# Performance work log

Hardware: AMD Instinct MI355X
Metric: run time of the kernel (lower is better)

## Reference

```python
import jax, jax.numpy as jnp
import numpy as np

DIM = 2048
N_HEADS = 16
HEAD_DIM = DIM // N_HEADS
ROPE_BASE = 10000


def l2norm(x, axis=-1, eps=1e-12):
    n = jnp.sqrt(jnp.sum(x * x, axis=axis, keepdims=True))
    return x / jnp.maximum(n, eps)


def rope_tables(T, dim, base, dtype):
    theta = 1.0 / (base ** (jnp.arange(0, dim, 2, dtype=dtype) / dim))  # [dim/2]
    ang = jnp.arange(T, dtype=dtype)[:, None] * theta[None, :]          # [T, dim/2]
    return jnp.sin(ang), jnp.cos(ang)


def apply_rope(x, sin, cos):
    # x: [B, H, T, D]; sin/cos: [T, D/2] (half-split convention, not interleaved)
    half = x.shape[-1] // 2
    xr, xi = x[..., :half], x[..., half:]
    yr = xr * cos - xi * sin
    yi = xr * sin + xi * cos
    return jnp.concatenate([yr, yi], axis=-1)


def setup_inputs() -> dict:
    key = jax.random.key(0)
    ks = jax.random.split(key, 5)
    B, T = 1, 2048
    x = jax.random.normal(ks[0], (B, T, DIM), dtype=jnp.float32)
    wq = jax.random.normal(ks[1], (DIM, DIM), dtype=jnp.float32) * 0.02
    wk = jax.random.normal(ks[2], (DIM, DIM), dtype=jnp.float32) * 0.02
    wv = jax.random.normal(ks[3], (DIM, DIM), dtype=jnp.float32) * 0.02
    wo = jax.random.normal(ks[4], (DIM, DIM), dtype=jnp.float32) * 0.02
    sqk = jnp.ones((N_HEADS, 1, HEAD_DIM), dtype=jnp.float32) * (1.0 / DIM ** 0.5)
    return {"x": x, "wq": wq, "wk": wk, "wv": wv, "wo": wo, "sqk": sqk}


def reference(x, wq, wk, wv, wo, sqk):
    B, T, C = x.shape
    H, D = N_HEADS, HEAD_DIM
    restore = C ** 0.5  # restore_scale_sqk = sqkinit / sqkscale
    actual_sqk = sqk * restore  # [H, 1, D]

    def proj(w):
        return jnp.einsum('btc,oc->bto', x, w).reshape(B, T, H, D).transpose(0, 2, 1, 3)

    q = proj(wq)  # [B, H, T, D]
    new_k = proj(wk)
    new_v = proj(wv)

    sin, cos = rope_tables(T, D, ROPE_BASE, x.dtype)
    q = apply_rope(q, sin, cos) * actual_sqk
    k = apply_rope(new_k, sin, cos) * actual_sqk

    # NOTE: original uses scale=head_dim**0.5 (multiplies by sqrt(D))
    scores = jnp.einsum('bhqd,bhkd->bhqk', q, k) * (D ** 0.5)
    mask = jnp.tril(jnp.ones((T, T), dtype=bool))
    scores = jnp.where(mask, scores, jnp.finfo(scores.dtype).min)
    attn = jax.nn.softmax(scores, axis=-1)
    out = jnp.einsum('bhqk,bhkd->bhqd', attn, new_v)  # [B, H, T, D]
    out = out.transpose(0, 2, 1, 3).reshape(B, T, C)
    out = jnp.einsum('btc,oc->bto', out, wo)
    return (l2norm(out), (new_k, new_v))
```

## Files before the change

### kernel.cpp

```cpp
#include <hip/hip_runtime.h>

typedef __bf16 bf16x8 __attribute__((ext_vector_type(8)));
typedef float f32x4 __attribute__((ext_vector_type(4)));
typedef unsigned short us4 __attribute__((ext_vector_type(4)));

constexpr int TT = 2048;
constexpr int CC = 2048;
constexpr int HH = 16;
constexpr int DD = 128;

__device__ __forceinline__ unsigned short f2bf(float f) {
  unsigned u = __builtin_bit_cast(unsigned, f);
  u += 0x7FFFu + ((u >> 16) & 1u);
  return (unsigned short)(u >> 16);
}
__device__ __forceinline__ float bf2f(unsigned short b) {
  unsigned u = ((unsigned)b) << 16;
  return __builtin_bit_cast(float, u);
}

__device__ __forceinline__ void gld_lds16(const unsigned short* g, unsigned short* l) {
  __builtin_amdgcn_global_load_lds(
      (const __attribute__((address_space(1))) unsigned int*)g,
      (__attribute__((address_space(3))) unsigned int*)l,
      16, 0, 0);
}

__global__ __launch_bounds__(256) void k_cvt5(
    const float* __restrict__ s0, const float* __restrict__ s1,
    const float* __restrict__ s2, const float* __restrict__ s3,
    const float* __restrict__ s4,
    unsigned short* __restrict__ d0, unsigned short* __restrict__ d1,
    unsigned short* __restrict__ d2, unsigned short* __restrict__ d3,
    unsigned short* __restrict__ d4) {
  const int m = blockIdx.y;
  const float* src = (m == 0) ? s0 : (m == 1) ? s1 : (m == 2) ? s2 : (m == 3) ? s3 : s4;
  unsigned short* dst = (m == 0) ? d0 : (m == 1) ? d1 : (m == 2) ? d2 : (m == 3) ? d3 : d4;
  int i = blockIdx.x * 256 + threadIdx.x;
  const float4* s = (const float4*)src;
  float4 a = s[2 * i], b = s[2 * i + 1];
  us4 lo = { f2bf(a.x), f2bf(a.y), f2bf(a.z), f2bf(a.w) };
  us4 hi = { f2bf(b.x), f2bf(b.y), f2bf(b.z), f2bf(b.w) };
  us4* d = (us4*)dst;
  d[2 * i] = lo;
  d[2 * i + 1] = hi;
}

#define WAIT_LGKM0                                      \
  asm volatile("s_waitcnt lgkmcnt(0)" ::: "memory");    \
  __builtin_amdgcn_sched_barrier(0);
#define BAR __builtin_amdgcn_s_barrier();

__global__ __launch_bounds__(512, 2) void k_gemm192(
    const unsigned short* __restrict__ A, const unsigned short* __restrict__ B,
    unsigned short* __restrict__ qraw,
    float* __restrict__ outk, float* __restrict__ outv) {
  __shared__ alignas(16) unsigned short As[2][256 * 64];
  __shared__ alignas(16) unsigned short Bs[2][192 * 64];
  const int K = CC, NT = K >> 6, NT2 = NT >> 1;
  const int tid = threadIdx.x;
  const int m0 = blockIdx.y * 256, n0 = blockIdx.x * 192;
  const int wid = tid >> 6, lane = tid & 63;
  const int wr = wid >> 2, wc = wid & 3;
  const int lr = lane & 15, lg = lane >> 4;

  auto stA = [&](int buf, int jb, int tile) {
#pragma unroll
    for (int j = jb; j < jb + 2; ++j) {
      const int ch = tid + j * 512;
      const int r = ch >> 3, c8 = ch & 7;
      gld_lds16(A + (size_t)(m0 + r) * K + tile * 64 + ((c8 ^ (r & 7)) * 8),
                &As[buf][ch * 8]);
    }
  };
  auto stB2 = [&](int buf, int tile) {
#pragma unroll
    for (int j = 0; j < 2; ++j) {
      const int ch = tid + j * 512;
      const int r = ch >> 3, c8 = ch & 7;
      gld_lds16(B + (size_t)(n0 + r) * K + tile * 64 + ((c8 ^ (r & 7)) * 8),
                &Bs[buf][ch * 8]);
    }
  };
  auto stB1 = [&](int buf, int tile) {
    const int ch = tid + 1024;
    const int r = ch >> 3, c8 = ch & 7;
    gld_lds16(B + (size_t)(n0 + r) * K + tile * 64 + ((c8 ^ (r & 7)) * 8),
              &Bs[buf][ch * 8]);
  };

  f32x4 acc[8][3] = {};
  bf16x8 alo[4][2], ahi[4][2], b01[2][2], b2v[2];

  auto rdAlo = [&](int d) {
#pragma unroll
    for (int im = 0; im < 4; ++im)
#pragma unroll
      for (int kk = 0; kk < 2; ++kk) {
        const int row = wr * 128 + im * 16 + lr;
        alo[im][kk] = *(const bf16x8*)(&As[d][row * 64 + (((kk * 4 + lg) ^ (row & 7)) * 8)]);
      }
  };
  auto rdAhi = [&](int d) {
#pragma unroll
    for (int im = 0; im < 4; ++im)
#pragma unroll
      for (int kk = 0; kk < 2; ++kk) {
        const int row = wr * 128 + (4 + im) * 16 + lr;
        ahi[im][kk] = *(const bf16x8*)(&As[d][row * 64 + (((kk * 4 + lg) ^ (row & 7)) * 8)]);
      }
  };
  auto rdB01 = [&](int d) {
#pragma unroll
    for (int in = 0; in < 2; ++in)
#pragma unroll
      for (int kk = 0; kk < 2; ++kk) {
        const int row = wc * 48 + in * 16 + lr;
        b01[in][kk] = *(const bf16x8*)(&Bs[d][row * 64 + (((kk * 4 + lg) ^ (row & 7)) * 8)]);
      }
  };
  auto rdB2 = [&](int d) {
#pragma unroll
    for (int kk = 0; kk < 2; ++kk) {
      const int row = wc * 48 + 32 + lr;
      b2v[kk] = *(const bf16x8*)(&Bs[d][row * 64 + (((kk * 4 + lg) ^ (row & 7)) * 8)]);
    }
  };

  auto q_lo01 = [&]() {
    __builtin_amdgcn_s_setprio(1);
#pragma unroll
    for (int im = 0; im < 4; ++im)
#pragma unroll
      for (int in = 0; in < 2; ++in)
#pragma unroll
        for (int kk = 0; kk < 2; ++kk)
          acc[im][in] = __builtin_amdgcn_mfma_f32_16x16x32_bf16(alo[im][kk], b01[in][kk], acc[im][in], 0, 0, 0);
    __builtin_amdgcn_s_setprio(0);
  };
  auto q_lo2 = [&]() {
    __builtin_amdgcn_s_setprio(1);
#pragma unroll
    for (int im = 0; im < 4; ++im)
#pragma unroll
      for (int kk = 0; kk < 2; ++kk)
        acc[im][2] = __builtin_amdgcn_mfma_f32_16x16x32_bf16(alo[im][kk], b2v[kk], acc[im][2], 0, 0, 0);
    __builtin_amdgcn_s_setprio(0);
  };
  auto q_hi2 = [&]() {
    __builtin_amdgcn_s_setprio(1);
#pragma unroll
    for (int im = 0; im < 4; ++im)
#pragma unroll
      for (int kk = 0; kk < 2; ++kk)
        acc[4 + im][2] = __builtin_amdgcn_mfma_f32_16x16x32_bf16(ahi[im][kk], b2v[kk], acc[4 + im][2], 0, 0, 0);
    __builtin_amdgcn_s_setprio(0);
  };
  auto q_hi01 = [&]() {
    __builtin_amdgcn_s_setprio(1);
#pragma unroll
    for (int im = 0; im < 4; ++im)
#pragma unroll
      for (int in = 0; in < 2; ++in)
#pragma unroll
        for (int kk = 0; kk < 2; ++kk)
          acc[4 + im][in] = __builtin_amdgcn_mfma_f32_16x16x32_bf16(ahi[im][kk], b01[in][kk], acc[4 + im][in], 0, 0, 0);
    __builtin_amdgcn_s_setprio(0);
  };

  stB2(0, 0); stB1(0, 0); stA(0, 0, 0); stA(0, 2, 0);
  stB2(1, 1); stB1(1, 1);
  asm volatile("s_waitcnt vmcnt(3)" ::: "memory");
  __builtin_amdgcn_sched_barrier(0);
  BAR

  for (int t = 0; t < NT2; ++t) {
    const int t1 = 2 * t + 1, t2 = 2 * t + 2, t3 = 2 * t + 3;
    const bool s2 = t2 < NT;

    rdAlo(0); rdB01(0);
    stA(1, 0, t1);
    BAR WAIT_LGKM0
    q_lo01();
    BAR
    rdB2(0);
    stA(1, 2, t1);
    BAR WAIT_LGKM0
    q_lo2();
    BAR
    rdAhi(0);
    if (s2) stB2(0, t2);
    BAR WAIT_LGKM0
    q_hi2();
    BAR
    if (s2) stB1(0, t2);
    q_hi01();
    if (s2) { asm volatile("s_waitcnt vmcnt(3)" ::: "memory"); }
    else    { asm volatile("s_waitcnt vmcnt(0)" ::: "memory"); }
    __builtin_amdgcn_sched_barrier(0);
    BAR

    rdAlo(1); rdB01(1);
    if (s2) stA(0, 0, t2);
    BAR WAIT_LGKM0
    q_lo01();
    BAR
    rdB2(1);
    if (s2) stA(0, 2, t2);
    BAR WAIT_LGKM0
    q_lo2();
    BAR
    rdAhi(1);
    if (s2) stB2(1, t3);
    BAR WAIT_LGKM0
    q_hi2();
    BAR
    if (s2) stB1(1, t3);
    q_hi01();
    if (s2) { asm volatile("s_waitcnt vmcnt(3)" ::: "memory"); }
    else    { asm volatile("s_waitcnt vmcnt(0)" ::: "memory"); }
    __builtin_amdgcn_sched_barrier(0);
    BAR
  }

#pragma unroll
  for (int mf = 0; mf < 8; ++mf) {
    const int row = m0 + wr * 128 + mf * 16 + lg * 4;
#pragma unroll
    for (int nf = 0; nf < 3; ++nf) {
      const int col = n0 + wc * 48 + nf * 16 + lr;
#pragma unroll
      for (int r = 0; r < 4; ++r) {
        float v = acc[mf][nf][r];
        int rr = row + r;
        if (col < 2048) {
          qraw[(size_t)rr * 2048 + col] = f2bf(v);
        } else if (col < 4096) {
          int c = col - 2048;
          outk[(size_t)(c >> 7) * (TT * DD) + (size_t)rr * DD + (c & 127)] = v;
        } else {
          int c = col - 4096;
          outv[(size_t)(c >> 7) * (TT * DD) + (size_t)rr * DD + (c & 127)] = v;
        }
      }
    }
  }
}

__global__ __launch_bounds__(512, 2) void k_gemm8p(
    const unsigned short* __restrict__ A, const unsigned short* __restrict__ B,
    int N, int K, int kspan,
    float* __restrict__ out0, float* __restrict__ out1,
    float* __restrict__ out2, float* __restrict__ out3) {
  __shared__ alignas(16) unsigned short As[2][2][128 * 64];
  __shared__ alignas(16) unsigned short Bs[2][2][128 * 64];
  const int tid = threadIdx.x;
  const int m0 = blockIdx.y * 256, n0 = blockIdx.x * 256;
  const int kbeg = blockIdx.z * kspan;
  const int NT = kspan >> 6, NT2 = NT >> 1;
  const int wid = tid >> 6, lane = tid & 63;
  const int wr = wid >> 2, wc = wid & 3;
  const int lr = lane & 15, lg = lane >> 4;
  const int bh = wc >> 1, brow0 = (wc & 1) * 64;

  const int sr0 = tid >> 3, sc0 = tid & 7;
  const unsigned short* Ab = A + kbeg;
  const unsigned short* Bb = B + kbeg;

  auto stageA = [&](int buf, int half, int tile) {
    const int koff = tile * 64;
#pragma unroll
    for (int j = 0; j < 2; ++j) {
      const int r = sr0 + j * 64;
      gld_lds16(Ab + (size_t)(m0 + half * 128 + r) * K + koff + ((sc0 ^ (r & 7)) * 8),
                &As[buf][half][(tid + j * 512) * 8]);
    }
  };
  auto stageB = [&](int buf, int half, int tile) {
    const int koff = tile * 64;
#pragma unroll
    for (int j = 0; j < 2; ++j) {
      const int r = sr0 + j * 64;
      gld_lds16(Bb + (size_t)(n0 + half * 128 + r) * K + koff + ((sc0 ^ (r & 7)) * 8),
                &Bs[buf][half][(tid + j * 512) * 8]);
    }
  };

  f32x4 acc[8][4] = {};
  bf16x8 alo[4][2], ahi[4][2], ba[2][2], bb[2][2];

  auto rdAlo = [&](int d) {
#pragma unroll
    for (int im = 0; im < 4; ++im)
#pragma unroll
      for (int kk = 0; kk < 2; ++kk) {
        const int row = im * 16 + lr;
        alo[im][kk] = *(const bf16x8*)(&As[d][wr][row * 64 + (((kk * 4 + lg) ^ (row & 7)) * 8)]);
      }
  };
  auto rdAhi = [&](int d) {
#pragma unroll
    for (int im = 0; im < 4; ++im)
#pragma unroll
      for (int kk = 0; kk < 2; ++kk) {
        const int row = (4 + im) * 16 + lr;
        ahi[im][kk] = *(const bf16x8*)(&As[d][wr][row * 64 + (((kk * 4 + lg) ^ (row & 7)) * 8)]);
      }
  };
  auto rdBa = [&](int d) {
#pragma unroll
    for (int in = 0; in < 2; ++in)
#pragma unroll
      for (int kk = 0; kk < 2; ++kk) {
        const int row = brow0 + in * 16 + lr;
        ba[in][kk] = *(const bf16x8*)(&Bs[d][bh][row * 64 + (((kk * 4 + lg) ^ (row & 7)) * 8)]);
      }
  };
  auto rdBb = [&](int d) {
#pragma unroll
    for (int in = 0; in < 2; ++in)
#pragma unroll
      for (int kk = 0; kk < 2; ++kk) {
        const int row = brow0 + (2 + in) * 16 + lr;
        bb[in][kk] = *(const bf16x8*)(&Bs[d][bh][row * 64 + (((kk * 4 + lg) ^ (row & 7)) * 8)]);
      }
  };

#define MFMA_Q(MB, NB, AF, BF)                                                     \
  __builtin_amdgcn_s_setprio(1);                                                   \
  _Pragma("unroll") for (int im = 0; im < 4; ++im)                                 \
      _Pragma("unroll") for (int in = 0; in < 2; ++in)                             \
          _Pragma("unroll") for (int kk = 0; kk < 2; ++kk)                         \
              acc[MB + im][NB + in] = __builtin_amdgcn_mfma_f32_16x16x32_bf16(     \
                  AF[im][kk], BF[in][kk], acc[MB + im][NB + in], 0, 0, 0);         \
  __builtin_amdgcn_s_setprio(0);

  stageB(0, 0, 0); stageB(0, 1, 0); stageA(0, 0, 0); stageA(0, 1, 0);
  if (NT > 1) { stageB(1, 0, 1); stageB(1, 1, 1); }
  asm volatile("s_waitcnt vmcnt(4)" ::: "memory");
  __builtin_amdgcn_sched_barrier(0);
  BAR

  for (int t = 0; t < NT2; ++t) {
    const int t1 = 2 * t + 1, t2 = 2 * t + 2, t3 = 2 * t + 3;
    const bool s2 = t2 < NT, s3 = t3 < NT;

    rdAlo(0); rdBa(0);
    stageA(1, 0, t1);
    BAR WAIT_LGKM0
    MFMA_Q(0, 0, alo, ba)
    BAR
    rdBb(0);
    stageA(1, 1, t1);
    BAR WAIT_LGKM0
    MFMA_Q(0, 2, alo, bb)
    BAR
    rdAhi(0);
    if (s2) stageB(0, 0, t2);
    BAR WAIT_LGKM0
    MFMA_Q(4, 2, ahi, bb)
    BAR
    if (s2) stageB(0, 1, t2);
    MFMA_Q(4, 0, ahi, ba)
    if (s2) { asm volatile("s_waitcnt vmcnt(4)" ::: "memory"); }
    else    { asm volatile("s_waitcnt vmcnt(0)" ::: "memory"); }
    __builtin_amdgcn_sched_barrier(0);
    BAR

    rdAlo(1); rdBa(1);
    if (s2) stageA(0, 0, t2);
    BAR WAIT_LGKM0
    MFMA_Q(0, 0, alo, ba)
    BAR
    rdBb(1);
    if (s2) stageA(0, 1, t2);
    BAR WAIT_LGKM0
    MFMA_Q(0, 2, alo, bb)
    BAR
    rdAhi(1);
    if (s3) stageB(1, 0, t3);
    BAR WAIT_LGKM0
    MFMA_Q(4, 2, ahi, bb)
    BAR
    if (s3) stageB(1, 1, t3);
    MFMA_Q(4, 0, ahi, ba)
    if (s3) { asm volatile("s_waitcnt vmcnt(4)" ::: "memory"); }
    else    { asm volatile("s_waitcnt vmcnt(0)" ::: "memory"); }
    __builtin_amdgcn_sched_barrier(0);
    BAR
  }
#undef MFMA_Q

  int z = blockIdx.z;
  float* dst = (z == 0) ? out0 : (z == 1) ? out1 : (z == 2) ? out2 : out3;
#pragma unroll
  for (int mf = 0; mf < 8; ++mf) {
    const int row = m0 + wr * 128 + mf * 16 + lg * 4;
#pragma unroll
    for (int nf = 0; nf < 4; ++nf) {
      const int col = n0 + wc * 64 + nf * 16 + lr;
#pragma unroll
      for (int r = 0; r < 4; ++r) {
        dst[(size_t)(row + r) * N + col] = acc[mf][nf][r];
      }
    }
  }
}
#undef WAIT_LGKM0
#undef BAR

__global__ __launch_bounds__(256) void k_rope(
    const unsigned short* __restrict__ qraw, const float* __restrict__ Kraw,
    const float* __restrict__ sqk,
    unsigned short* __restrict__ qb, unsigned short* __restrict__ kb) {
  const int t = blockIdx.x;
  for (int i = threadIdx.x; i < HH * 64; i += 256) {
    int h = i >> 6, dp = i & 63;
    float theta = expf(-(float)dp * 0.14391156831212787f);
    float ang = (float)t * theta;
    float sn, cs;
    sincosf(ang, &sn, &cs);
    float qr = bf2f(qraw[(size_t)t * CC + h * DD + dp]);
    float qi = bf2f(qraw[(size_t)t * CC + h * DD + dp + 64]);
    const float* kp = Kraw + (size_t)h * TT * DD + (size_t)t * DD;
    float kr = kp[dp], ki = kp[dp + 64];
    float sr = sqk[h * DD + dp];
    float si = sqk[h * DD + dp + 64];
    float qsr = sr * 512.0f, qsi = si * 512.0f;
    float ksr = sr * 45.25483399593904f, ksi = si * 45.25483399593904f;
    unsigned short* qo = qb + ((size_t)h * TT + t) * DD;
    unsigned short* ko = kb + ((size_t)h * TT + t) * DD;
    qo[dp]      = f2bf((qr * cs - qi * sn) * qsr);
    qo[dp + 64] = f2bf((qr * sn + qi * cs) * qsi);
    ko[dp]      = f2bf((kr * cs - ki * sn) * ksr);
    ko[dp + 64] = f2bf((kr * sn + ki * cs) * ksi);
  }
}

__global__ __launch_bounds__(256) void k_vt(
    const float* __restrict__ Vraw, unsigned short* __restrict__ vt) {
  const int h = blockIdx.z;
  const int t0 = blockIdx.x * 64, d0 = blockIdx.y * 64;
  __shared__ unsigned short tile[64][65];
  const float* vp = Vraw + (size_t)h * TT * DD;
  for (int i = threadIdx.x; i < 4096; i += 256) {
    int r = i >> 6, c = i & 63;
    tile[r][c] = f2bf(vp[(size_t)(t0 + r) * DD + d0 + c]);
  }
  __syncthreads();
  unsigned short* op = vt + (size_t)h * DD * TT;
  for (int i = threadIdx.x; i < 4096; i += 256) {
    int dr = i >> 6, tc = i & 63;
    op[(size_t)(d0 + dr) * TT + t0 + tc] = tile[tc][dr];
  }
}

__global__ __launch_bounds__(512) void k_attn_pair(
    const unsigned short* __restrict__ qb, const unsigned short* __restrict__ kb,
    const unsigned short* __restrict__ vt, unsigned short* __restrict__ ob) {
  const int gA = blockIdx.x, h = blockIdx.y;
  const int gB = 31 - gA;
  const int ntiles = gB + 1;
  const int tid = threadIdx.x;
  const int wid = tid >> 6, lane = tid & 63;
  const int lr = lane & 15, lg = lane >> 4;
  const int gq = (wid >> 2) ? gB : gA;
  const int q0 = gq * 64 + (wid & 3) * 16;

  __shared__ alignas(16) unsigned short Ks[2][64 * 128];
  __shared__ alignas(16) unsigned short Vs[2][128 * 64];
  __shared__ alignas(16) unsigned short P[8][16][72];

  const unsigned short* qh = qb + (size_t)h * TT * DD;
  const unsigned short* kh = kb + (size_t)h * TT * DD;
  const unsigned short* vh = vt + (size_t)h * DD * TT;

  auto stageKV = [&](int buf, int kt) {
    const int k0 = kt * 64;
#pragma unroll
    for (int half = 0; half < 2; ++half) {
      int ch = tid + half * 512;
      int r = ch >> 4, c4 = ch & 15;
      gld_lds16(kh + (size_t)(k0 + r) * DD + ((c4 ^ (r & 7)) * 8), Ks[buf] + ch * 8);
    }
#pragma unroll
    for (int half = 0; half < 2; ++half) {
      int ch = tid + half * 512;
      int d = ch >> 3, c8 = ch & 7;
      gld_lds16(vh + (size_t)d * TT + k0 + ((c8 ^ (d & 7)) * 8), Vs[buf] + ch * 8);
    }
  };

  bf16x8 qf[4];
#pragma unroll
  for (int c = 0; c < 4; ++c)
    qf[c] = *(const bf16x8*)(qh + (size_t)(q0 + lr) * DD + c * 32 + lg * 8);

  f32x4 acc[8] = {};
  float mrow[4] = {-3e38f, -3e38f, -3e38f, -3e38f};
  float lsum[4] = {0.f, 0.f, 0.f, 0.f};

  stageKV(0, 0);
  asm volatile("s_waitcnt vmcnt(0)" ::: "memory");
  __builtin_amdgcn_sched_barrier(0);
  __builtin_amdgcn_s_barrier();

  for (int kt = 0; kt < ntiles; ++kt) {
    const int cur = kt & 1;
    const int k0 = kt * 64;
    if (kt + 1 < ntiles) stageKV(cur ^ 1, kt + 1);

    if (k0 <= q0 + 15) {
      f32x4 sv[4] = {};
#pragma unroll
      for (int ktile = 0; ktile < 4; ++ktile) {
        const int row = ktile * 16 + lr;
#pragma unroll
        for (int c = 0; c < 4; ++c) {
          int chn = (c * 4 + lg) ^ (lr & 7);
          bf16x8 kf = *(const bf16x8*)(Ks[cur] + row * 128 + chn * 8);
          sv[ktile] = __builtin_amdgcn_mfma_f32_16x16x32_bf16(qf[c], kf, sv[ktile], 0, 0, 0);
        }
      }
      if (k0 + 63 > q0) {
#pragma unroll
        for (int ktile = 0; ktile < 4; ++ktile)
#pragma unroll
          for (int r = 0; r < 4; ++r) {
            int key = k0 + ktile * 16 + lr;
            int qrow = q0 + lg * 4 + r;
            if (key > qrow) sv[ktile][r] = -1e30f;
          }
      }
      float pmax[4];
#pragma unroll
      for (int r = 0; r < 4; ++r)
        pmax[r] = fmaxf(fmaxf(sv[0][r], sv[1][r]), fmaxf(sv[2][r], sv[3][r]));
#pragma unroll
      for (int msk = 1; msk <= 8; msk <<= 1)
#pragma unroll
        for (int r = 0; r < 4; ++r) pmax[r] = fmaxf(pmax[r], __shfl_xor(pmax[r], msk));
      float p[4][4], ps[4], scl[4];
#pragma unroll
      for (int r = 0; r < 4; ++r) {
        float mn = fmaxf(mrow[r], pmax[r]);
        scl[r] = __expf(mrow[r] - mn);
        mrow[r] = mn;
        ps[r] = 0.f;
#pragma unroll
        for (int ktile = 0; ktile < 4; ++ktile) {
          p[ktile][r] = __expf(sv[ktile][r] - mn);
          ps[r] += p[ktile][r];
        }
      }
#pragma unroll
      for (int msk = 1; msk <= 8; msk <<= 1)
#pragma unroll
        for (int r = 0; r < 4; ++r) ps[r] += __shfl_xor(ps[r], msk);
#pragma unroll
      for (int r = 0; r < 4; ++r) lsum[r] = lsum[r] * scl[r] + ps[r];
#pragma unroll
      for (int n = 0; n < 8; ++n)
#pragma unroll
        for (int r = 0; r < 4; ++r) acc[n][r] *= scl[r];
#pragma unroll
      for (int ktile = 0; ktile < 4; ++ktile)
#pragma unroll
        for (int r = 0; r < 4; ++r)
          P[wid][lg * 4 + r][ktile * 16 + lr] = f2bf(p[ktile][r]);
      asm volatile("s_waitcnt lgkmcnt(0)" ::: "memory");
      __builtin_amdgcn_sched_barrier(0);
      bf16x8 pf[2];
#pragma unroll
      for (int ks = 0; ks < 2; ++ks)
        pf[ks] = *(const bf16x8*)(&P[wid][lr][ks * 32 + lg * 8]);
#pragma unroll
      for (int n = 0; n < 8; ++n) {
        const int row = n * 16 + lr;
#pragma unroll
        for (int ks = 0; ks < 2; ++ks) {
          int chn = (ks * 4 + lg) ^ (lr & 7);
          bf16x8 vf = *(const bf16x8*)(Vs[cur] + row * 64 + chn * 8);
          acc[n] = __builtin_amdgcn_mfma_f32_16x16x32_bf16(pf[ks], vf, acc[n], 0, 0, 0);
        }
      }
    }
    asm volatile("s_waitcnt vmcnt(0)" ::: "memory");
    __builtin_amdgcn_sched_barrier(0);
    __builtin_amdgcn_s_barrier();
  }

  float inv[4];
#pragma unroll
  for (int r = 0; r < 4; ++r) inv[r] = 1.0f / lsum[r];
#pragma unroll
  for (int n = 0; n < 8; ++n)
#pragma unroll
    for (int r = 0; r < 4; ++r) {
      int t = q0 + lg * 4 + r;
      ob[(size_t)t * CC + h * DD + n * 16 + lr] = f2bf(acc[n][r] * inv[r]);
    }
}

__global__ __launch_bounds__(256) void k_l2norm(
    const float* __restrict__ Of0, const float* __restrict__ Of1,
    const float* __restrict__ Of2, const float* __restrict__ Of3,
    float* __restrict__ out) {
  const int t = blockIdx.x;
  const int tid = threadIdx.x;
  const float4* p0 = (const float4*)(Of0 + (size_t)t * CC);
  const float4* p1 = (const float4*)(Of1 + (size_t)t * CC);
  const float4* p2 = (const float4*)(Of2 + (size_t)t * CC);
  const float4* p3 = (const float4*)(Of3 + (size_t)t * CC);
  float4 a = p0[2 * tid], b = p0[2 * tid + 1];
  float4 a1 = p1[2 * tid], b1 = p1[2 * tid + 1];
  float4 a2 = p2[2 * tid], b2 = p2[2 * tid + 1];
  float4 a3 = p3[2 * tid], b3 = p3[2 * tid + 1];
  a.x += a1.x + a2.x + a3.x; a.y += a1.y + a2.y + a3.y;
  a.z += a1.z + a2.z + a3.z; a.w += a1.w + a2.w + a3.w;
  b.x += b1.x + b2.x + b3.x; b.y += b1.y + b2.y + b3.y;
  b.z += b1.z + b2.z + b3.z; b.w += b1.w + b2.w + b3.w;
  float ss = a.x * a.x + a.y * a.y + a.z * a.z + a.w * a.w +
             b.x * b.x + b.y * b.y + b.z * b.z + b.w * b.w;
#pragma unroll
  for (int msk = 1; msk < 64; msk <<= 1) ss += __shfl_xor(ss, msk);
  __shared__ float red[4];
  if ((tid & 63) == 0) red[tid >> 6] = ss;
  __syncthreads();
  ss = red[0] + red[1] + red[2] + red[3];
  float sc = 1.0f / fmaxf(sqrtf(ss), 1e-12f);
  float4 oa = { a.x * sc, a.y * sc, a.z * sc, a.w * sc };
  float4 obv = { b.x * sc, b.y * sc, b.z * sc, b.w * sc };
  float4* o = (float4*)(out + (size_t)t * CC);
  o[2 * tid] = oa;
  o[2 * tid + 1] = obv;
}

extern "C" void kernel_launch(void* const* d_in, const int* in_sizes, int n_in,
                              void* d_out, int out_size, void* d_ws, size_t ws_size,
                              hipStream_t stream) {
  const float* x   = (const float*)d_in[0];
  const float* wq  = (const float*)d_in[1];
  const float* wk  = (const float*)d_in[2];
  const float* wv  = (const float*)d_in[3];
  const float* wo  = (const float*)d_in[4];
  const float* sqk = (const float*)d_in[5];

  float* out_norm = (float*)d_out;
  float* out_k = out_norm + (size_t)4 * 1024 * 1024;
  float* out_v = out_norm + (size_t)8 * 1024 * 1024;

  char* ws = (char*)d_ws;
  unsigned short* xb  = (unsigned short*)(ws);
  unsigned short* w1b = (unsigned short*)(ws + (8u << 20));
  unsigned short* wob = (unsigned short*)(ws + (32u << 20));
  unsigned short* qb  = (unsigned short*)(ws + (40u << 20));
  unsigned short* kb  = (unsigned short*)(ws + (48u << 20));
  unsigned short* vtb = (unsigned short*)(ws + (56u << 20));
  unsigned short* obb = (unsigned short*)(ws + (64u << 20));
  unsigned short* qraw = (unsigned short*)(ws + (72u << 20));

  float* Of0 = (float*)(ws + (72u << 20));
  float* Of1 = (float*)(ws);
  float* Of2 = (float*)(ws + (16u << 20));
  float* Of3 = (float*)(ws + (40u << 20));

  k_cvt5<<<dim3(2048, 5), 256, 0, stream>>>(
      x, wq, wk, wv, wo,
      xb, w1b, w1b + (size_t)4 * 1024 * 1024, w1b + (size_t)8 * 1024 * 1024, wob);

  k_gemm192<<<dim3(32, 8), 512, 0, stream>>>(xb, w1b, qraw, out_k, out_v);

  k_rope<<<TT, 256, 0, stream>>>(qraw, out_k, sqk, qb, kb);
  k_vt<<<dim3(32, 2, 16), 256, 0, stream>>>(out_v, vtb);

  k_attn_pair<<<dim3(16, 16), 512, 0, stream>>>(qb, kb, vtb, obb);

  k_gemm8p<<<dim3(8, 8, 4), 512, 0, stream>>>(obb, wob, CC, CC, CC / 4,
                                              Of0, Of1, Of2, Of3);

  k_l2norm<<<TT, 256, 0, stream>>>(Of0, Of1, Of2, Of3, out_norm);
}
```

Baseline: 201.8 us.

## Fuse V transpose into QKV GEMM epilogue and store split-K partials in bf16

```diff
diff --git a/kernel.cpp b/kernel.cpp
--- a/kernel.cpp
+++ b/kernel.cpp
@@ -54,7 +54,8 @@
 __global__ __launch_bounds__(512, 2) void k_gemm192(
     const unsigned short* __restrict__ A, const unsigned short* __restrict__ B,
     unsigned short* __restrict__ qraw,
-    float* __restrict__ outk, float* __restrict__ outv) {
+    float* __restrict__ outk, float* __restrict__ outv,
+    unsigned short* __restrict__ vtb) {
   __shared__ alignas(16) unsigned short As[2][256 * 64];
   __shared__ alignas(16) unsigned short Bs[2][192 * 64];
   const int K = CC, NT = K >> 6, NT2 = NT >> 1;
@@ -229,19 +230,26 @@
 #pragma unroll
     for (int nf = 0; nf < 3; ++nf) {
       const int col = n0 + wc * 48 + nf * 16 + lr;
-#pragma unroll
-      for (int r = 0; r < 4; ++r) {
-        float v = acc[mf][nf][r];
-        int rr = row + r;
-        if (col < 2048) {
-          qraw[(size_t)rr * 2048 + col] = f2bf(v);
-        } else if (col < 4096) {
-          int c = col - 2048;
-          outk[(size_t)(c >> 7) * (TT * DD) + (size_t)rr * DD + (c & 127)] = v;
-        } else {
-          int c = col - 4096;
-          outv[(size_t)(c >> 7) * (TT * DD) + (size_t)rr * DD + (c & 127)] = v;
+      if (col < 2048) {
+#pragma unroll
+        for (int r = 0; r < 4; ++r)
+          qraw[(size_t)(row + r) * 2048 + col] = f2bf(acc[mf][nf][r]);
+      } else if (col < 4096) {
+        const int c = col - 2048;
+#pragma unroll
+        for (int r = 0; r < 4; ++r)
+          outk[(size_t)(c >> 7) * (TT * DD) + (size_t)(row + r) * DD + (c & 127)] = acc[mf][nf][r];
+      } else {
+        const int c = col - 4096;
+        const int hh = c >> 7, d2 = c & 127;
+        us4 tv;
+#pragma unroll
+        for (int r = 0; r < 4; ++r) {
+          float v = acc[mf][nf][r];
+          outv[(size_t)hh * (TT * DD) + (size_t)(row + r) * DD + d2] = v;
+          tv[r] = f2bf(v);
         }
+        *(us4*)(vtb + (size_t)hh * (size_t)(DD * TT) + (size_t)d2 * TT + row) = tv;
       }
     }
   }
@@ -250,8 +258,8 @@
 __global__ __launch_bounds__(512, 2) void k_gemm8p(
     const unsigned short* __restrict__ A, const unsigned short* __restrict__ B,
     int N, int K, int kspan,
-    float* __restrict__ out0, float* __restrict__ out1,
-    float* __restrict__ out2, float* __restrict__ out3) {
+    unsigned short* __restrict__ out0, unsigned short* __restrict__ out1,
+    unsigned short* __restrict__ out2, unsigned short* __restrict__ out3) {
   __shared__ alignas(16) unsigned short As[2][2][128 * 64];
   __shared__ alignas(16) unsigned short Bs[2][2][128 * 64];
   const int tid = threadIdx.x;
@@ -392,7 +400,7 @@
 #undef MFMA_Q
 
   int z = blockIdx.z;
-  float* dst = (z == 0) ? out0 : (z == 1) ? out1 : (z == 2) ? out2 : out3;
+  unsigned short* dst = (z == 0) ? out0 : (z == 1) ? out1 : (z == 2) ? out2 : out3;
 #pragma unroll
   for (int mf = 0; mf < 8; ++mf) {
     const int row = m0 + wr * 128 + mf * 16 + lg * 4;
@@ -401,7 +409,7 @@
       const int col = n0 + wc * 64 + nf * 16 + lr;
 #pragma unroll
       for (int r = 0; r < 4; ++r) {
-        dst[(size_t)(row + r) * N + col] = acc[mf][nf][r];
+        dst[(size_t)(row + r) * N + col] = f2bf(acc[mf][nf][r]);
       }
     }
   }
@@ -437,24 +445,6 @@
   }
 }
 
-__global__ __launch_bounds__(256) void k_vt(
-    const float* __restrict__ Vraw, unsigned short* __restrict__ vt) {
-  const int h = blockIdx.z;
-  const int t0 = blockIdx.x * 64, d0 = blockIdx.y * 64;
-  __shared__ unsigned short tile[64][65];
-  const float* vp = Vraw + (size_t)h * TT * DD;
-  for (int i = threadIdx.x; i < 4096; i += 256) {
-    int r = i >> 6, c = i & 63;
-    tile[r][c] = f2bf(vp[(size_t)(t0 + r) * DD + d0 + c]);
-  }
-  __syncthreads();
-  unsigned short* op = vt + (size_t)h * DD * TT;
-  for (int i = threadIdx.x; i < 4096; i += 256) {
-    int dr = i >> 6, tc = i & 63;
-    op[(size_t)(d0 + dr) * TT + t0 + tc] = tile[tc][dr];
-  }
-}
-
 __global__ __launch_bounds__(512) void k_attn_pair(
     const unsigned short* __restrict__ qb, const unsigned short* __restrict__ kb,
     const unsigned short* __restrict__ vt, unsigned short* __restrict__ ob) {
@@ -603,25 +593,23 @@
 }
 
 __global__ __launch_bounds__(256) void k_l2norm(
-    const float* __restrict__ Of0, const float* __restrict__ Of1,
-    const float* __restrict__ Of2, const float* __restrict__ Of3,
+    const unsigned short* __restrict__ Of0, const unsigned short* __restrict__ Of1,
+    const unsigned short* __restrict__ Of2, const unsigned short* __restrict__ Of3,
     float* __restrict__ out) {
   const int t = blockIdx.x;
   const int tid = threadIdx.x;
-  const float4* p0 = (const float4*)(Of0 + (size_t)t * CC);
-  const float4* p1 = (const float4*)(Of1 + (size_t)t * CC);
-  const float4* p2 = (const float4*)(Of2 + (size_t)t * CC);
-  const float4* p3 = (const float4*)(Of3 + (size_t)t * CC);
-  float4 a = p0[2 * tid], b = p0[2 * tid + 1];
-  float4 a1 = p1[2 * tid], b1 = p1[2 * tid + 1];
-  float4 a2 = p2[2 * tid], b2 = p2[2 * tid + 1];
-  float4 a3 = p3[2 * tid], b3 = p3[2 * tid + 1];
-  a.x += a1.x + a2.x + a3.x; a.y += a1.y + a2.y + a3.y;
-  a.z += a1.z + a2.z + a3.z; a.w += a1.w + a2.w + a3.w;
-  b.x += b1.x + b2.x + b3.x; b.y += b1.y + b2.y + b3.y;
-  b.z += b1.z + b2.z + b3.z; b.w += b1.w + b2.w + b3.w;
-  float ss = a.x * a.x + a.y * a.y + a.z * a.z + a.w * a.w +
-             b.x * b.x + b.y * b.y + b.z * b.z + b.w * b.w;
+  const size_t base = (size_t)t * CC + tid * 8;
+  bf16x8 a0 = *(const bf16x8*)(Of0 + base);
+  bf16x8 a1 = *(const bf16x8*)(Of1 + base);
+  bf16x8 a2 = *(const bf16x8*)(Of2 + base);
+  bf16x8 a3 = *(const bf16x8*)(Of3 + base);
+  float v[8];
+  float ss = 0.f;
+#pragma unroll
+  for (int j = 0; j < 8; ++j) {
+    v[j] = (float)a0[j] + (float)a1[j] + (float)a2[j] + (float)a3[j];
+    ss += v[j] * v[j];
+  }
 #pragma unroll
   for (int msk = 1; msk < 64; msk <<= 1) ss += __shfl_xor(ss, msk);
   __shared__ float red[4];
@@ -629,11 +617,11 @@
   __syncthreads();
   ss = red[0] + red[1] + red[2] + red[3];
   float sc = 1.0f / fmaxf(sqrtf(ss), 1e-12f);
-  float4 oa = { a.x * sc, a.y * sc, a.z * sc, a.w * sc };
-  float4 obv = { b.x * sc, b.y * sc, b.z * sc, b.w * sc };
-  float4* o = (float4*)(out + (size_t)t * CC);
-  o[2 * tid] = oa;
-  o[2 * tid + 1] = obv;
+  float4 oa = { v[0] * sc, v[1] * sc, v[2] * sc, v[3] * sc };
+  float4 obv = { v[4] * sc, v[5] * sc, v[6] * sc, v[7] * sc };
+  float4* o = (float4*)(out + base);
+  o[0] = oa;
+  o[1] = obv;
 }
 
 extern "C" void kernel_launch(void* const* d_in, const int* in_sizes, int n_in,
@@ -660,19 +648,18 @@
   unsigned short* obb = (unsigned short*)(ws + (64u << 20));
   unsigned short* qraw = (unsigned short*)(ws + (72u << 20));
 
-  float* Of0 = (float*)(ws + (72u << 20));
-  float* Of1 = (float*)(ws);
-  float* Of2 = (float*)(ws + (16u << 20));
-  float* Of3 = (float*)(ws + (40u << 20));
+  unsigned short* Of0 = (unsigned short*)(ws + (72u << 20));
+  unsigned short* Of1 = (unsigned short*)(ws);
+  unsigned short* Of2 = (unsigned short*)(ws + (8u << 20));
+  unsigned short* Of3 = (unsigned short*)(ws + (16u << 20));
 
   k_cvt5<<<dim3(2048, 5), 256, 0, stream>>>(
       x, wq, wk, wv, wo,
       xb, w1b, w1b + (size_t)4 * 1024 * 1024, w1b + (size_t)8 * 1024 * 1024, wob);
 
-  k_gemm192<<<dim3(32, 8), 512, 0, stream>>>(xb, w1b, qraw, out_k, out_v);
+  k_gemm192<<<dim3(32, 8), 512, 0, stream>>>(xb, w1b, qraw, out_k, out_v, vtb);
 
   k_rope<<<TT, 256, 0, stream>>>(qraw, out_k, sqk, qb, kb);
-  k_vt<<<dim3(32, 2, 16), 256, 0, stream>>>(out_v, vtb);
 
   k_attn_pair<<<dim3(16, 16), 512, 0, stream>>>(qb, kb, vtb, obb);
 
```

Measured after the change: 191.2 us. 5.2% less time.
